# Optimization experiments

Hardware: AMD Instinct MI355X
Metric: run time of the kernel (lower is better)

Reference implementation:

```python
import jax, jax.numpy as jnp
import numpy as np

HIDDEN = 1152
HEADS = 16
HEAD_DIM = HIDDEN // HEADS

def setup_inputs() -> dict:
    key = jax.random.key(0)
    ks = jax.random.split(key, 7)
    s = 1.0 / np.sqrt(HIDDEN)
    return {
        "x": jax.random.normal(ks[0], (16, 1024, HIDDEN), dtype=jnp.float32),
        "w_qkv": jax.random.normal(ks[1], (3 * HIDDEN, HIDDEN), dtype=jnp.float32) * s,
        "b_qkv": jax.random.normal(ks[2], (3 * HIDDEN,), dtype=jnp.float32) * 0.01,
        "q_gamma": jnp.ones((HEAD_DIM,), dtype=jnp.float32),
        "k_gamma": jnp.ones((HEAD_DIM,), dtype=jnp.float32),
        "w_proj": jax.random.normal(ks[3], (HIDDEN, HIDDEN), dtype=jnp.float32) * s,
        "b_proj": jax.random.normal(ks[4], (HIDDEN,), dtype=jnp.float32) * 0.01,
    }

def _rmsnorm(t, gamma):
    # normalize over last dim (head_dim); torch RMSNorm default eps = finfo(dtype).eps
    eps = jnp.asarray(jnp.finfo(t.dtype).eps, t.dtype)
    ms = jnp.mean(jnp.square(t), axis=-1, keepdims=True)
    return t * jax.lax.rsqrt(ms + eps) * gamma

def reference(x, w_qkv, b_qkv, q_gamma, k_gamma, w_proj, b_proj):
    B, S, H = x.shape
    qkv = x @ w_qkv.T + b_qkv                       # [B,S,3H]
    qkv = qkv.reshape(B, S, 3, HEADS, HEAD_DIM)
    qkv = jnp.transpose(qkv, (2, 0, 3, 1, 4))       # [3,B,nh,S,hd]
    q, k, v = qkv[0], qkv[1], qkv[2]
    q = _rmsnorm(q, q_gamma)
    k = _rmsnorm(k, k_gamma)
    scale = 1.0 / np.sqrt(HEAD_DIM)
    scores = jnp.einsum('bhqd,bhkd->bhqk', q, k) * scale
    probs = jax.nn.softmax(scores, axis=-1)
    out = jnp.einsum('bhqk,bhkd->bhqd', probs, v)   # [B,nh,S,hd]
    out = jnp.transpose(out, (0, 2, 1, 3)).reshape(B, S, H)
    return out @ w_proj.T + b_proj
```

## Files before the change

kernel.cpp:

```cpp
#include <hip/hip_runtime.h>

typedef _Float16 f16;
typedef _Float16 f16x8 __attribute__((ext_vector_type(8)));
typedef _Float16 f16x4 __attribute__((ext_vector_type(4)));
typedef float f32x4 __attribute__((ext_vector_type(4)));

__device__ __forceinline__ void gld16(const void* g, void* l) {
    __builtin_amdgcn_global_load_lds(
        (const __attribute__((address_space(1))) void*)g,
        (__attribute__((address_space(3))) void*)l,
        16, 0, 0);
}

__global__ __launch_bounds__(256) void f32_to_f16_vec(const float* __restrict__ in,
                                                      f16* __restrict__ out, long n4) {
    long i = (long)blockIdx.x * 256 + threadIdx.x;
    if (i < n4) {
        float4 v = ((const float4*)in)[i];
        f16x4 o = {(f16)v.x, (f16)v.y, (f16)v.z, (f16)v.w};
        ((f16x4*)out)[i] = o;
    }
}

constexpr int GEMM_BUF_E = 12288;

struct GPtrs {
    const f16 *a0, *a1, *a2, *a3, *b0, *b1;
};

__device__ __forceinline__ void stage6(f16* s, const GPtrs& g, int dA, int dB) {
    gld16(g.a0, s + dA);
    gld16(g.a1, s + dA + 2048);
    gld16(g.a2, s + dA + 4096);
    gld16(g.a3, s + dA + 6144);
    gld16(g.b0, s + dB);
    gld16(g.b1, s + dB + 2048);
}

template<int BUF, bool STG>
__device__ __forceinline__ void tile_step(f16* sm, GPtrs& g,
                                          int dA, int dB,
                                          int offA, int offB,
                                          f32x4 (&acc)[8][4]) {
    const f16* bp = sm + BUF * GEMM_BUF_E;
    if (STG) {
        constexpr int SB = (BUF + 2) % 3;
        stage6(sm + SB * GEMM_BUF_E, g, dA, dB);
        g.a0 += 32; g.a1 += 32; g.a2 += 32; g.a3 += 32;
        g.b0 += 32; g.b1 += 32;
    }
    f16x8 bf[4], af[4], ag[4];
#pragma unroll
    for (int nt = 0; nt < 4; ++nt) bf[nt] = *(const f16x8*)(bp + offB + nt * 512);
#pragma unroll
    for (int mt = 0; mt < 4; ++mt) af[mt] = *(const f16x8*)(bp + offA + mt * 512);
#pragma unroll
    for (int mt = 0; mt < 4; ++mt) ag[mt] = *(const f16x8*)(bp + offA + 2048 + mt * 512);
    __builtin_amdgcn_s_setprio(1);
#pragma unroll
    for (int mt = 0; mt < 4; ++mt)
#pragma unroll
        for (int nt = 0; nt < 4; ++nt)
            acc[mt][nt] = __builtin_amdgcn_mfma_f32_16x16x32_f16(
                af[mt], bf[nt], acc[mt][nt], 0, 0, 0);
#pragma unroll
    for (int mt = 0; mt < 4; ++mt)
#pragma unroll
        for (int nt = 0; nt < 4; ++nt)
            acc[4 + mt][nt] = __builtin_amdgcn_mfma_f32_16x16x32_f16(
                ag[mt], bf[nt], acc[4 + mt][nt], 0, 0, 0);
    __builtin_amdgcn_s_setprio(0);
}

__global__ __launch_bounds__(256, 2) void gemm8(const f16* __restrict__ A,
                                                const f16* __restrict__ B,
                                                const float* __restrict__ bias,
                                                float* __restrict__ Cf,
                                                f16* __restrict__ Ch,
                                                int M, int N, int K) {
    __shared__ f16 sm[3 * GEMM_BUF_E];
    const int tid = threadIdx.x;
    const int w = tid >> 6, lane = tid & 63;
    const int quad = lane >> 4, l16 = lane & 15;
    const int wm = w >> 1, wn = w & 1;

    const int nnb = N >> 7;
    const int mpx = (M >> 8) >> 3;
    const int xcd = blockIdx.x & 7;
    const int s = blockIdx.x >> 3;
    const int mband = s / nnb;
    const int nblk = s - mband * nnb;
    const long m0 = (long)(xcd * mpx + mband) << 8;
    const long n0 = (long)nblk << 7;

    const int r4 = lane >> 2;
    const int sc = ((lane & 3) ^ ((lane >> 3) & 3)) << 3;
    GPtrs g;
    g.a0 = A + (m0 +   0 + w * 16 + r4) * (long)K + sc;
    g.a1 = A + (m0 +  64 + w * 16 + r4) * (long)K + sc;
    g.a2 = A + (m0 + 128 + w * 16 + r4) * (long)K + sc;
    g.a3 = A + (m0 + 192 + w * 16 + r4) * (long)K + sc;
    g.b0 = B + (n0 +   0 + w * 16 + r4) * (long)K + sc;
    g.b1 = B + (n0 +  64 + w * 16 + r4) * (long)K + sc;
    const int dA = __builtin_amdgcn_readfirstlane(w * 512);
    const int dB = __builtin_amdgcn_readfirstlane(8192 + w * 512);

    const int swz = (quad ^ ((l16 >> 1) & 3)) << 3;
    const int offA = (wm * 128 + l16) * 32 + swz;
    const int offB = 8192 + (wn * 64 + l16) * 32 + swz;

    f32x4 acc[8][4] = {};

    stage6(sm, g, dA, dB);
    {
        GPtrs g1 = g;
        g1.a0 += 32; g1.a1 += 32; g1.a2 += 32; g1.a3 += 32; g1.b0 += 32; g1.b1 += 32;
        stage6(sm + GEMM_BUF_E, g1, dA, dB);
    }
    g.a0 += 64; g.a1 += 64; g.a2 += 64; g.a3 += 64; g.b0 += 64; g.b1 += 64;
    asm volatile("s_waitcnt vmcnt(6)" ::: "memory");
    __builtin_amdgcn_s_barrier();
    __builtin_amdgcn_sched_barrier(0);

#define VMB(NSTR) asm volatile("s_waitcnt vmcnt(" NSTR ")" ::: "memory"); \
                  __builtin_amdgcn_s_barrier();                           \
                  __builtin_amdgcn_sched_barrier(0);

#pragma unroll 1
    for (int it = 0; it < 11; ++it) {
        tile_step<0, true>(sm, g, dA, dB, offA, offB, acc); VMB("6")
        tile_step<1, true>(sm, g, dA, dB, offA, offB, acc); VMB("6")
        tile_step<2, true>(sm, g, dA, dB, offA, offB, acc); VMB("6")
    }
    tile_step<0, true >(sm, g, dA, dB, offA, offB, acc); VMB("6")
    tile_step<1, false>(sm, g, dA, dB, offA, offB, acc); VMB("0")
    tile_step<2, false>(sm, g, dA, dB, offA, offB, acc);
#undef VMB

    float bv[4];
#pragma unroll
    for (int nt = 0; nt < 4; ++nt)
        bv[nt] = bias ? bias[n0 + wn * 64 + nt * 16 + l16] : 0.f;
#pragma unroll
    for (int mt = 0; mt < 8; ++mt) {
#pragma unroll
        for (int r = 0; r < 4; ++r) {
            const long row = m0 + wm * 128 + mt * 16 + quad * 4 + r;
#pragma unroll
            for (int nt = 0; nt < 4; ++nt) {
                const long col = n0 + wn * 64 + nt * 16 + l16;
                const float v = acc[mt][nt][r] + bv[nt];
                if (Ch) Ch[row * (long)N + col] = (f16)v;
                else    Cf[row * (long)N + col] = v;
            }
        }
    }
}

__global__ __launch_bounds__(256) void qk_norm2(f16* __restrict__ qkv,
                                                const float* __restrict__ qg,
                                                const float* __restrict__ kg,
                                                f16* __restrict__ kc) {
    const float QSCALE = 0.117851130198f;
    const int t = blockIdx.x * 256 + threadIdx.x;
    const int h = t & 15;
    const long bs = t >> 4;
    f16* qp = qkv + bs * 3456 + h * 72;
    {
        f16x8 v[9];
        float ss = 0.f;
#pragma unroll
        for (int c = 0; c < 9; ++c) {
            v[c] = *(const f16x8*)(qp + c * 8);
#pragma unroll
            for (int j = 0; j < 8; ++j) { float f = (float)v[c][j]; ss += f * f; }
        }
        const float rs = rsqrtf(ss * (1.f / 72.f) + 1.1920928955078125e-7f) * QSCALE;
#pragma unroll
        for (int c = 0; c < 9; ++c) {
            f16x8 o;
#pragma unroll
            for (int j = 0; j < 8; ++j) o[j] = (f16)((float)v[c][j] * rs * qg[c * 8 + j]);
            *(f16x8*)(qp + c * 8) = o;
        }
    }
    {
        const f16* kp = qp + 1152;
        f16* dst = kc + ((long)((bs >> 10) * 16 + h) * 1024 + (bs & 1023)) * 72;
        f16x8 v[9];
        float ss = 0.f;
#pragma unroll
        for (int c = 0; c < 9; ++c) {
            v[c] = *(const f16x8*)(kp + c * 8);
#pragma unroll
            for (int j = 0; j < 8; ++j) { float f = (float)v[c][j]; ss += f * f; }
        }
        const float rs = rsqrtf(ss * (1.f / 72.f) + 1.1920928955078125e-7f);
#pragma unroll
        for (int c = 0; c < 9; ++c) {
            f16x8 o;
#pragma unroll
            for (int j = 0; j < 8; ++j) o[j] = (f16)((float)v[c][j] * rs * kg[c * 8 + j]);
            *(f16x8*)(dst + c * 8) = o;
        }
    }
}

__global__ __launch_bounds__(256) void vt_kernel(const f16* __restrict__ QKV,
                                                 f16* __restrict__ Vt) {
    __shared__ f16 tile[64][73];
    const int tid = threadIdx.x;
    const int bh = blockIdx.x;
    const int b = bh >> 4, h = bh & 15;
    const int s0 = blockIdx.y * 64;
    for (int idx = tid; idx < 64 * 72; idx += 256) {
        const int r = idx / 72, c = idx % 72;
        tile[r][c] = QKV[((long)(b * 1024 + s0 + r)) * 3456 + 2304 + h * 72 + c];
    }
    __syncthreads();
    for (int idx = tid; idx < 72 * 64; idx += 256) {
        const int d = idx >> 6, s = idx & 63;
        Vt[((long)bh * 72 + d) * 1024 + s0 + s] = tile[s][d];
    }
}

__global__ __launch_bounds__(256) void attn2(const f16* __restrict__ QKV,
                                             const f16* __restrict__ Kc,
                                             const f16* __restrict__ Vt,
                                             f16* __restrict__ O) {
    constexpr int S = 1024;
    __shared__ f16 smem[64 * 72 + 80 * 76];
    f16* Ks = smem;
    f16* Vs = smem + 64 * 72;
    const int tid = threadIdx.x;
    const int w = tid >> 6, lane = tid & 63;
    const int quad = lane >> 4, l16 = lane & 15;

    const int b = blockIdx.x;
    const int xcd = b & 7;
    const int j = b >> 3;
    const int bh = ((j >> 3) << 3) | xcd;
    const int qt = j & 7;
    const int bb = bh >> 4, h = bh & 15;
    const int q0 = qt * 128;

    for (int i = tid; i < 8 * 76; i += 256) {
        const int pr = i / 76, pc = i % 76;
        Vs[(72 + pr) * 76 + pc] = (pr == 0 && pc < 64) ? (f16)1.f : (f16)0.f;
    }

    const f16* qrow0 = QKV + ((long)(bb * 1024 + q0 + w * 32 + l16)) * 3456 + h * 72;
    const f16* qrow1 = qrow0 + (long)16 * 3456;
    f16x8 qz = {};
    f16x8 qf[2][3];
    qf[0][0] = *(const f16x8*)(qrow0 + quad * 8);
    qf[0][1] = *(const f16x8*)(qrow0 + 32 + quad * 8);
    qf[0][2] = (quad == 0) ? *(const f16x8*)(qrow0 + 64) : qz;
    qf[1][0] = *(const f16x8*)(qrow1 + quad * 8);
    qf[1][1] = *(const f16x8*)(qrow1 + 32 + quad * 8);
    qf[1][2] = (quad == 0) ? *(const f16x8*)(qrow1 + 64) : qz;

    f32x4 o[2][5] = {};

    const f16* gK = Kc + (long)bh * S * 72;
    const f16* gV = Vt + (long)bh * 72 * S;

    for (int s0 = 0; s0 < S; s0 += 64) {
        for (int ch = w; ch < 9; ch += 4)
            gld16(gK + (long)s0 * 72 + ch * 512 + lane * 8,
                  &Ks[__builtin_amdgcn_readfirstlane(ch * 512)]);
#pragma unroll
        for (int it = 0; it < 3; ++it) {
            const int idx = it * 256 + tid;
            if (idx < 576) {
                const int d = idx >> 3, s8 = (idx & 7) * 8;
                f16x8 v = *(const f16x8*)(gV + (long)d * 1024 + s0 + s8);
                f16x4 lo = {v[0], v[1], v[2], v[3]};
                f16x4 hi = {v[4], v[5], v[6], v[7]};
                *(f16x4*)&Vs[d * 76 + s8] = lo;
                *(f16x4*)&Vs[d * 76 + s8 + 4] = hi;
            }
        }
        __syncthreads();

        f32x4 sc[4][2] = {};
#pragma unroll
        for (int ss = 0; ss < 4; ++ss) {
            const int base = (ss * 16 + l16) * 72;
            f16x8 k0 = *(const f16x8*)&Ks[base + quad * 8];
            f16x8 k1 = *(const f16x8*)&Ks[base + 32 + quad * 8];
            f16x8 k2 = *(const f16x8*)&Ks[base + 64 + quad * 8];
            sc[ss][0] = __builtin_amdgcn_mfma_f32_16x16x32_f16(k0, qf[0][0], sc[ss][0], 0, 0, 0);
            sc[ss][0] = __builtin_amdgcn_mfma_f32_16x16x32_f16(k1, qf[0][1], sc[ss][0], 0, 0, 0);
            sc[ss][0] = __builtin_amdgcn_mfma_f32_16x16x32_f16(k2, qf[0][2], sc[ss][0], 0, 0, 0);
            sc[ss][1] = __builtin_amdgcn_mfma_f32_16x16x32_f16(k0, qf[1][0], sc[ss][1], 0, 0, 0);
            sc[ss][1] = __builtin_amdgcn_mfma_f32_16x16x32_f16(k1, qf[1][1], sc[ss][1], 0, 0, 0);
            sc[ss][1] = __builtin_amdgcn_mfma_f32_16x16x32_f16(k2, qf[1][2], sc[ss][1], 0, 0, 0);
        }

        f16x4 pf[4][2];
#pragma unroll
        for (int ss = 0; ss < 4; ++ss)
#pragma unroll
            for (int qs = 0; qs < 2; ++qs) {
                f16x4 pk;
#pragma unroll
                for (int r = 0; r < 4; ++r) pk[r] = (f16)__expf(sc[ss][qs][r]);
                pf[ss][qs] = pk;
            }

#pragma unroll
        for (int vt = 0; vt < 5; ++vt) {
#pragma unroll
            for (int ss = 0; ss < 4; ++ss) {
                f16x4 vf = *(const f16x4*)&Vs[(vt * 16 + l16) * 76 + ss * 16 + quad * 4];
                o[0][vt] = __builtin_amdgcn_mfma_f32_16x16x16f16(vf, pf[ss][0], o[0][vt], 0, 0, 0);
                o[1][vt] = __builtin_amdgcn_mfma_f32_16x16x16f16(vf, pf[ss][1], o[1][vt], 0, 0, 0);
            }
        }
        __syncthreads();
    }

    const float l0 = __shfl(o[0][4][0], 32 + l16);
    const float l1 = __shfl(o[1][4][0], 32 + l16);
    const float inv[2] = {1.f / l0, 1.f / l1};

    f16* es = smem + w * 2560;
#pragma unroll
    for (int qs = 0; qs < 2; ++qs) {
        f16* row = es + (qs * 16 + l16) * 80;
#pragma unroll
        for (int vt = 0; vt < 5; ++vt)
#pragma unroll
            for (int r = 0; r < 4; ++r) {
                const int d = vt * 16 + quad * 4 + r;
                if (d < 72) row[d] = (f16)(o[qs][vt][r] * inv[qs]);
            }
    }
    const long rowbase = (long)bb * 1024 + q0 + w * 32;
#pragma unroll
    for (int it = 0; it < 5; ++it) {
        const int idx = it * 64 + lane;
        if (idx < 288) {
            const int q = idx / 9, c = idx - q * 9;
            f16x4 a = *(const f16x4*)&es[q * 80 + c * 8];
            f16x4 b2 = *(const f16x4*)&es[q * 80 + c * 8 + 4];
            f16* dst = O + (rowbase + q) * 1152 + h * 72 + c * 8;
            *(f16x4*)dst = a;
            *(f16x4*)(dst + 4) = b2;
        }
    }
}

extern "C" void kernel_launch(void* const* d_in, const int* in_sizes, int n_in,
                              void* d_out, int out_size, void* d_ws, size_t ws_size,
                              hipStream_t stream) {
    const float* x       = (const float*)d_in[0];
    const float* w_qkv   = (const float*)d_in[1];
    const float* b_qkv   = (const float*)d_in[2];
    const float* q_gamma = (const float*)d_in[3];
    const float* k_gamma = (const float*)d_in[4];
    const float* w_proj  = (const float*)d_in[5];
    const float* b_proj  = (const float*)d_in[6];
    float* out = (float*)d_out;

    char* p = (char*)d_ws;
    f16* x_h = (f16*)p;      p += (size_t)16384 * 1152 * 2;
    f16* wqkv_h = (f16*)p;   p += (size_t)3456 * 1152 * 2;
    f16* wproj_h = (f16*)p;  p += (size_t)1152 * 1152 * 2;
    f16* qkv_h = (f16*)p;    p += (size_t)16384 * 3456 * 2;
    const size_t needed = (size_t)(p - (char*)d_ws);
    if (ws_size < needed) return;

    f16* k_c = (f16*)d_out;
    f16* v_t = (f16*)d_out + (size_t)16384 * 1152;

    f32_to_f16_vec<<<18432, 256, 0, stream>>>(x, x_h, 16384L * 1152 / 4);
    f32_to_f16_vec<<<3888, 256, 0, stream>>>(w_qkv, wqkv_h, 3456L * 1152 / 4);
    f32_to_f16_vec<<<1296, 256, 0, stream>>>(w_proj, wproj_h, 1152L * 1152 / 4);

    gemm8<<<1728, 256, 0, stream>>>(
        x_h, wqkv_h, b_qkv, nullptr, qkv_h, 16384, 3456, 1152);

    qk_norm2<<<1024, 256, 0, stream>>>(qkv_h, q_gamma, k_gamma, k_c);
    vt_kernel<<<dim3(256, 16), 256, 0, stream>>>(qkv_h, v_t);

    attn2<<<2048, 256, 0, stream>>>(qkv_h, k_c, v_t, x_h );

    gemm8<<<576, 256, 0, stream>>>(
        x_h, wproj_h, b_proj, out, nullptr, 16384, 1152, 1152);
}
```

Baseline: 523.2 us.

## Double-buffer K/V tiles in attention kernel with register-staged V prefetch

Splits the attention kernel's shared-memory K and V tiles into two buffers. The next tile's K load (direct-to-LDS) and V load (into registers) are issued before the current tile's MFMA work, and the V registers are written to the alternate buffer afterwards, so global latency overlaps compute and one barrier per iteration is dropped. It also raises wave priority around the MFMA sections. The cost is double the LDS footprint and extra registers, which may reduce occupancy.

```diff
diff --git a/kernel.cpp b/kernel.cpp
--- a/kernel.cpp
+++ b/kernel.cpp
@@ -229,9 +229,11 @@
                                              const f16* __restrict__ Vt,
                                              f16* __restrict__ O) {
     constexpr int S = 1024;
-    __shared__ f16 smem[64 * 72 + 80 * 76];
-    f16* Ks = smem;
-    f16* Vs = smem + 64 * 72;
+    constexpr int KSZ = 64 * 72;
+    constexpr int VSZ = 80 * 76;
+    __shared__ f16 smem[2 * KSZ + 2 * VSZ];
+    f16* KsA = smem;
+    f16* VsA = smem + 2 * KSZ;
     const int tid = threadIdx.x;
     const int w = tid >> 6, lane = tid & 63;
     const int quad = lane >> 4, l16 = lane & 15;
@@ -246,7 +248,9 @@
 
     for (int i = tid; i < 8 * 76; i += 256) {
         const int pr = i / 76, pc = i % 76;
-        Vs[(72 + pr) * 76 + pc] = (pr == 0 && pc < 64) ? (f16)1.f : (f16)0.f;
+        const f16 pv = (pr == 0 && pc < 64) ? (f16)1.f : (f16)0.f;
+        VsA[(72 + pr) * 76 + pc] = pv;
+        VsA[VSZ + (72 + pr) * 76 + pc] = pv;
     }
 
     const f16* qrow0 = QKV + ((long)(bb * 1024 + q0 + w * 32 + l16)) * 3456 + h * 72;
@@ -265,25 +269,51 @@
     const f16* gK = Kc + (long)bh * S * 72;
     const f16* gV = Vt + (long)bh * 72 * S;
 
-    for (int s0 = 0; s0 < S; s0 += 64) {
-        for (int ch = w; ch < 9; ch += 4)
-            gld16(gK + (long)s0 * 72 + ch * 512 + lane * 8,
-                  &Ks[__builtin_amdgcn_readfirstlane(ch * 512)]);
-#pragma unroll
-        for (int it = 0; it < 3; ++it) {
-            const int idx = it * 256 + tid;
-            if (idx < 576) {
-                const int d = idx >> 3, s8 = (idx & 7) * 8;
-                f16x8 v = *(const f16x8*)(gV + (long)d * 1024 + s0 + s8);
-                f16x4 lo = {v[0], v[1], v[2], v[3]};
-                f16x4 hi = {v[4], v[5], v[6], v[7]};
-                *(f16x4*)&Vs[d * 76 + s8] = lo;
-                *(f16x4*)&Vs[d * 76 + s8 + 4] = hi;
-            }
-        }
-        __syncthreads();
+    f16x8 vr[3];
+
+    for (int ch = w; ch < 9; ch += 4)
+        gld16(gK + ch * 512 + lane * 8,
+              &KsA[__builtin_amdgcn_readfirstlane(ch * 512)]);
+#pragma unroll
+    for (int it = 0; it < 3; ++it) {
+        const int idx = it * 256 + tid;
+        if (idx < 576)
+            vr[it] = *(const f16x8*)(gV + (long)(idx >> 3) * 1024 + (idx & 7) * 8);
+    }
+#pragma unroll
+    for (int it = 0; it < 3; ++it) {
+        const int idx = it * 256 + tid;
+        if (idx < 576) {
+            const int d = idx >> 3, s8 = (idx & 7) * 8;
+            f16x4 lo = {vr[it][0], vr[it][1], vr[it][2], vr[it][3]};
+            f16x4 hi = {vr[it][4], vr[it][5], vr[it][6], vr[it][7]};
+            *(f16x4*)&VsA[d * 76 + s8] = lo;
+            *(f16x4*)&VsA[d * 76 + s8 + 4] = hi;
+        }
+    }
+    __syncthreads();
+
+#pragma unroll 1
+    for (int t = 0; t < 16; ++t) {
+        const int buf = t & 1;
+        const f16* Ks = KsA + buf * KSZ;
+        const f16* Vs = VsA + buf * VSZ;
+
+        if (t < 15) {
+            const int s1 = (t + 1) * 64;
+            for (int ch = w; ch < 9; ch += 4)
+                gld16(gK + (long)s1 * 72 + ch * 512 + lane * 8,
+                      &KsA[__builtin_amdgcn_readfirstlane((buf ^ 1) * KSZ + ch * 512)]);
+#pragma unroll
+            for (int it = 0; it < 3; ++it) {
+                const int idx = it * 256 + tid;
+                if (idx < 576)
+                    vr[it] = *(const f16x8*)(gV + (long)(idx >> 3) * 1024 + s1 + (idx & 7) * 8);
+            }
+        }
 
         f32x4 sc[4][2] = {};
+        __builtin_amdgcn_s_setprio(1);
 #pragma unroll
         for (int ss = 0; ss < 4; ++ss) {
             const int base = (ss * 16 + l16) * 72;
@@ -297,6 +327,7 @@
             sc[ss][1] = __builtin_amdgcn_mfma_f32_16x16x32_f16(k1, qf[1][1], sc[ss][1], 0, 0, 0);
             sc[ss][1] = __builtin_amdgcn_mfma_f32_16x16x32_f16(k2, qf[1][2], sc[ss][1], 0, 0, 0);
         }
+        __builtin_amdgcn_s_setprio(0);
 
         f16x4 pf[4][2];
 #pragma unroll
@@ -309,6 +340,7 @@
                 pf[ss][qs] = pk;
             }
 
+        __builtin_amdgcn_s_setprio(1);
 #pragma unroll
         for (int vt = 0; vt < 5; ++vt) {
 #pragma unroll
@@ -316,6 +348,21 @@
                 f16x4 vf = *(const f16x4*)&Vs[(vt * 16 + l16) * 76 + ss * 16 + quad * 4];
                 o[0][vt] = __builtin_amdgcn_mfma_f32_16x16x16f16(vf, pf[ss][0], o[0][vt], 0, 0, 0);
                 o[1][vt] = __builtin_amdgcn_mfma_f32_16x16x16f16(vf, pf[ss][1], o[1][vt], 0, 0, 0);
+            }
+        }
+        __builtin_amdgcn_s_setprio(0);
+
+        if (t < 15) {
+#pragma unroll
+            for (int it = 0; it < 3; ++it) {
+                const int idx = it * 256 + tid;
+                if (idx < 576) {
+                    const int d = idx >> 3, s8 = (idx & 7) * 8;
+                    f16x4 lo = {vr[it][0], vr[it][1], vr[it][2], vr[it][3]};
+                    f16x4 hi = {vr[it][4], vr[it][5], vr[it][6], vr[it][7]};
+                    *(f16x4*)&VsA[(buf ^ 1) * VSZ + d * 76 + s8] = lo;
+                    *(f16x4*)&VsA[(buf ^ 1) * VSZ + d * 76 + s8 + 4] = hi;
+                }
             }
         }
         __syncthreads();
```

After: 516.2 us. Within noise of the previous version (-1.3%).
